# Optimization experiments

Measured on AMD Instinct MI355X. Metric: run time of the kernel, lower is better.

Reference implementation:

```python
import jax, jax.numpy as jnp
import numpy as np

N_NODES = 100000
N_EDGES = 1600000
D_FEAT = 64
D_OUT = 64


def setup_inputs() -> dict:
    key = jax.random.key(0)
    ks = jax.random.split(key, 8)
    return {
        "feat": jax.random.normal(ks[0], (N_NODES, D_FEAT), dtype=jnp.float32),
        "emb": jax.random.normal(ks[1], (N_NODES, D_OUT), dtype=jnp.float32),
        "W1": jax.random.normal(ks[2], (D_OUT, D_FEAT), dtype=jnp.float32) * 0.1,
        "b1": jax.random.normal(ks[3], (D_OUT,), dtype=jnp.float32) * 0.1,
        "W2": jax.random.normal(ks[4], (D_OUT, D_OUT), dtype=jnp.float32) * 0.1,
        "b2": jax.random.normal(ks[5], (D_OUT,), dtype=jnp.float32) * 0.1,
        "edge_src": jax.random.randint(ks[6], (N_EDGES,), 0, N_NODES, dtype=jnp.int32),
        "edge_dst": jax.random.randint(ks[7], (N_EDGES,), 0, N_NODES, dtype=jnp.int32),
    }


def reference(feat, emb, W1, b1, W2, b2, edge_src, edge_dst):
    # n2v: per-node neighbor embedding sum (vectorized gather + segment-sum)
    n_nodes = feat.shape[0]
    nbr_sum = jax.ops.segment_sum(emb[edge_src], edge_dst, num_segments=n_nodes)  # [N, D_OUT]
    new_emb = jax.nn.relu(feat @ W1.T + b1 + nbr_sum @ W2.T + b2)  # [N, D_OUT]
    # g2v: graph embedding = sum of node embeddings
    graph_emb = new_emb.sum(axis=0)  # [D_OUT]
    return graph_emb
```

## Files before the change

kernel.cpp:

```cpp
#include <hip/hip_runtime.h>

#define N_NODES 100000
#define N_EDGES 1600000
#define D 64
#define CAP 32
#define OVF_CAP 8192
#define N_TILES 1563
#define NR 8
#define SLICE_EDGES 2048
#define N_SLICES 782
#define R1_BLOCKS 64
#define R1_ROWS 25
#define ASTRIDE 136

#define NB2 782
#define BCAP2 2560
#define EPB 8192
#define P1_BLOCKS 196
#define CVT_BLOCKS 64

typedef int    vint4  __attribute__((ext_vector_type(4)));
typedef short  s16x4  __attribute__((ext_vector_type(4)));
typedef short  s16x8  __attribute__((ext_vector_type(8)));
typedef float  f32x2  __attribute__((ext_vector_type(2)));
typedef float  f32x4  __attribute__((ext_vector_type(4)));
typedef __bf16 bf16x8 __attribute__((ext_vector_type(8)));

__device__ inline short f2bf(float f) {
    unsigned u = __builtin_bit_cast(unsigned, f);
    u += 0x7fffu + ((u >> 16) & 1u);
    return (short)(u >> 16);
}
__device__ inline s16x4 f2bf4(float4 v) {
    s16x4 r; r.x = f2bf(v.x); r.y = f2bf(v.y); r.z = f2bf(v.z); r.w = f2bf(v.w);
    return r;
}

#define WS_SLOTS_OFF 401408
#define WS_ACC_OFF   13201408
#define WS_OVFC_OFF  38801408
#define WS_OVF_OFF   38801424
#define WS_PART_OFF  38867200
#define WS_PART2_OFF 39267328
#define WS_EMB16_OFF 39283712
#define WS_NEEDED    (WS_PART2_OFF + R1_BLOCKS * 64 * 4)
#define WS_NEEDED16  (WS_EMB16_OFF + N_NODES * D * 2)

__global__ __launch_bounds__(512) void part_kernel(
    const int* __restrict__ edge_src, const int* __restrict__ edge_dst,
    int* __restrict__ bcnt, int* __restrict__ bkt,
    int* __restrict__ ovf_cnt, int2* __restrict__ ovf,
    const float* __restrict__ emb, unsigned* __restrict__ emb8) {
    const int tid = threadIdx.x;
    if (blockIdx.x >= P1_BLOCKS) {
        const float4* e4 = (const float4*)emb;
        const unsigned t0 = (blockIdx.x - P1_BLOCKS) * 512 + tid;
        for (unsigned j = t0; j < (unsigned)(N_NODES * D / 4);
             j += CVT_BLOCKS * 512) {
            float4 v = e4[j];
            int w = 0;
            w = __builtin_amdgcn_cvt_pk_fp8_f32(v.x, v.y, w, false);
            w = __builtin_amdgcn_cvt_pk_fp8_f32(v.z, v.w, w, true);
            emb8[j] = (unsigned)w;
        }
        return;
    }

    __shared__ int stage[EPB];
    __shared__ unsigned short bid[EPB];
    __shared__ int scA[1024];
    __shared__ int scB[1024];
    __shared__ int hist[NB2];
    int* const cur   = scB;
    int* const gbase = scA;

    const int e0 = blockIdx.x * EPB;
    for (int i = tid; i < NB2; i += 512) hist[i] = 0;
    __syncthreads();

    int ss[16], dd[16];
#pragma unroll
    for (int i = 0; i < 16; ++i) {
        const int e = e0 + i * 512 + tid;
        if (e < N_EDGES) { ss[i] = edge_src[e]; dd[i] = edge_dst[e]; }
        else             { ss[i] = 0; dd[i] = -1; }
    }

#pragma unroll
    for (int i = 0; i < 16; ++i)
        if (dd[i] >= 0) atomicAdd(&hist[dd[i] >> 7], 1);
    __syncthreads();

    scA[tid]       = (tid < NB2) ? hist[tid] : 0;
    scA[tid + 512] = 0;
    if (tid + 512 < NB2) scA[tid + 512] = hist[tid + 512];
    __syncthreads();
    {
        int* sA = scA;
        int* sB = scB;
        for (int off = 1; off < 1024; off <<= 1) {
            const int i1 = tid + 512;
            const int v0 = sA[tid] + ((tid >= off) ? sA[tid - off] : 0);
            const int v1 = sA[i1] + sA[i1 - off];
            sB[tid] = v0; sB[i1] = v1;
            __syncthreads();
            int* t = sA; sA = sB; sB = t;
        }
    }
    const int tot = scA[NB2 - 1];
    for (int i = tid; i < NB2; i += 512) cur[i] = scA[i] - hist[i];
    __syncthreads();

#pragma unroll
    for (int i = 0; i < 16; ++i) {
        if (dd[i] >= 0) {
            const int b = dd[i] >> 7;
            const int pos = atomicAdd(&cur[b], 1);
            stage[pos] = (ss[i] << 7) | (dd[i] & 127);
            bid[pos] = (unsigned short)b;
        }
    }
    for (int i = tid; i < NB2; i += 512)
        gbase[i] = atomicAdd(&bcnt[i], hist[i]);
    __syncthreads();

    for (int j = tid; j < tot; j += 512) {
        const int pk = stage[j];
        const int b  = bid[j];
        const int gpos = gbase[b] + (j - (cur[b] - hist[b]));
        if (gpos < BCAP2) {
            bkt[b * BCAP2 + gpos] = pk;
        } else {
            int oj = atomicAdd(ovf_cnt, 1);
            if (oj < OVF_CAP) ovf[oj] = make_int2(pk >> 7, (b << 7) | (pk & 127));
        }
    }
}

__global__ __launch_bounds__(512) void fill2_kernel(
    const int* __restrict__ bcnt, const int* __restrict__ bkt,
    int* __restrict__ cnt, int* __restrict__ slots,
    int* __restrict__ ovf_cnt, int2* __restrict__ ovf) {
    __shared__ int lcnt[128];
    const int b = blockIdx.x;
    const int tid = threadIdx.x;
    if (tid < 128) lcnt[tid] = 0;
    __syncthreads();
    int n = bcnt[b];
    if (n > BCAP2) n = BCAP2;
    for (int i = tid; i < n; i += 512) {
        const int pk = bkt[b * BCAP2 + i];
        const int dl = pk & 127;
        const int pos = atomicAdd(&lcnt[dl], 1);
        const int v = (b << 7) | dl;
        if (pos < CAP) {
            slots[v * CAP + pos] = pk >> 7;
        } else {
            int j = atomicAdd(ovf_cnt, 1);
            if (j < OVF_CAP) ovf[j] = make_int2(pk >> 7, v);
        }
    }
    __syncthreads();
    if (tid < 128) {
        const int v = (b << 7) | tid;
        if (v < N_NODES) cnt[v] = lcnt[tid];
    }
}

__global__ __launch_bounds__(256) void gather8_kernel(
    const unsigned* __restrict__ emb8, const int* __restrict__ cnt,
    const int* __restrict__ slots, float* __restrict__ acc) {
    const int lane = threadIdx.x & 63;
    const int wave = threadIdx.x >> 6;
    const int v = blockIdx.x * 4 + wave;
    const int q = lane >> 4;
    const int c = lane & 15;
    int deg = cnt[v];
    if (deg > CAP) deg = CAP;
    const int si = slots[v * CAP + (lane & (CAP - 1))];

    float4 sum = make_float4(0.f, 0.f, 0.f, 0.f);
    for (int e = 0; e < deg; e += 8) {
        const int i0 = e + q, i1 = e + 4 + q;
        const int s0 = __shfl(si, i0 & (CAP - 1));
        const int s1 = __shfl(si, i1 & (CAP - 1));
        unsigned x0 = 0u, x1 = 0u;
        if (i0 < deg) x0 = emb8[(unsigned)s0 * 16 + c];
        if (i1 < deg) x1 = emb8[(unsigned)s1 * 16 + c];
        const f32x2 a0 = __builtin_amdgcn_cvt_pk_f32_fp8((int)x0, false);
        const f32x2 a1 = __builtin_amdgcn_cvt_pk_f32_fp8((int)x0, true);
        const f32x2 b0 = __builtin_amdgcn_cvt_pk_f32_fp8((int)x1, false);
        const f32x2 b1 = __builtin_amdgcn_cvt_pk_f32_fp8((int)x1, true);
        sum.x += a0.x + b0.x;
        sum.y += a0.y + b0.y;
        sum.z += a1.x + b1.x;
        sum.w += a1.y + b1.y;
    }
#pragma unroll
    for (int off = 16; off < 64; off <<= 1) {
        sum.x += __shfl_xor(sum.x, off);
        sum.y += __shfl_xor(sum.y, off);
        sum.z += __shfl_xor(sum.z, off);
        sum.w += __shfl_xor(sum.w, off);
    }
    if (q == 0) {
        ((float4*)acc)[v * 16 + c] = sum;
    }
}

__global__ __launch_bounds__(256) void fill_kernel(
    const int* __restrict__ edge_src, const int* __restrict__ edge_dst,
    int* __restrict__ cnt, int* __restrict__ slots,
    int* __restrict__ ovf_cnt, int2* __restrict__ ovf) {
    const int r = blockIdx.x & (NR - 1);
    if (r == 7) return;
    const int slice = blockIdx.x >> 3;
    const int base_e = slice * SLICE_EDGES + threadIdx.x * 8;
    if (base_e >= N_EDGES) return;
    const vint4* s4 = (const vint4*)(edge_src + base_e);
    const vint4* d4 = (const vint4*)(edge_dst + base_e);
    vint4 a0 = __builtin_nontemporal_load(s4);
    vint4 a1 = __builtin_nontemporal_load(s4 + 1);
    vint4 b0 = __builtin_nontemporal_load(d4);
    vint4 b1 = __builtin_nontemporal_load(d4 + 1);
    int ss[8] = {a0.x, a0.y, a0.z, a0.w, a1.x, a1.y, a1.z, a1.w};
    int dd[8] = {b0.x, b0.y, b0.z, b0.w, b1.x, b1.y, b1.z, b1.w};
    int pos[8];
#pragma unroll
    for (int i = 0; i < 8; ++i) {
        pos[i] = ((dd[i] >> 14) == r) ? atomicAdd(&cnt[dd[i]], 1) : -1;
    }
#pragma unroll
    for (int i = 0; i < 8; ++i) {
        if (pos[i] >= 0 && pos[i] < CAP) slots[dd[i] * CAP + pos[i]] = ss[i];
    }
#pragma unroll
    for (int i = 0; i < 8; ++i) {
        if (pos[i] >= CAP) {
            int j = atomicAdd(ovf_cnt, 1);
            if (j < OVF_CAP) ovf[j] = make_int2(ss[i], dd[i]);
        }
    }
}

__global__ __launch_bounds__(256) void gather_kernel(
    const float* __restrict__ emb, const int* __restrict__ cnt,
    const int* __restrict__ slots, float* __restrict__ acc) {
    const int lane = threadIdx.x & 63;
    const int wave = threadIdx.x >> 6;
    const int v = blockIdx.x * 4 + wave;
    const int q  = lane >> 4;
    const int c4 = lane & 15;
    int deg = cnt[v];
    if (deg > CAP) deg = CAP;
    const int si = slots[v * CAP + (lane & (CAP - 1))];
    const float4* emb4 = (const float4*)emb;

    float4 sum = make_float4(0.f, 0.f, 0.f, 0.f);
    for (int e = 0; e < deg; e += 4) {
        const int idx = e + q;
        const int s = __shfl(si, idx & (CAP - 1));
        if (idx < deg) {
            float4 a = emb4[s * 16 + c4];
            sum.x += a.x; sum.y += a.y; sum.z += a.z; sum.w += a.w;
        }
    }
#pragma unroll
    for (int off = 16; off < 64; off <<= 1) {
        sum.x += __shfl_xor(sum.x, off);
        sum.y += __shfl_xor(sum.y, off);
        sum.z += __shfl_xor(sum.z, off);
        sum.w += __shfl_xor(sum.w, off);
    }
    if (q == 0) {
        ((float4*)acc)[v * 16 + c4] = sum;
    }
}

__global__ __launch_bounds__(256) void ovf_kernel(
    const float* __restrict__ emb, const int* __restrict__ ovf_cnt,
    const int2* __restrict__ ovf, float* __restrict__ acc) {
    int n = *ovf_cnt;
    if (n > OVF_CAP) n = OVF_CAP;
    const int lane = threadIdx.x & 63;
    const int wv = (blockIdx.x * 256 + threadIdx.x) >> 6;
    const int nwaves = (gridDim.x * 256) >> 6;
    for (int i = wv; i < n; i += nwaves) {
        int2 e = ovf[i];
        unsafeAtomicAdd(&acc[e.y * D + lane], emb[e.x * D + lane]);
    }
}

__global__ __launch_bounds__(256) void scatter_kernel(
    const float* __restrict__ emb,
    const int* __restrict__ edge_src, const int* __restrict__ edge_dst,
    float* __restrict__ acc) {
    int gid = blockIdx.x * 256 + threadIdx.x;
    int e = gid >> 6;
    int c = gid & 63;
    unsafeAtomicAdd(&acc[edge_dst[e] * D + c], emb[edge_src[e] * D + c]);
}

__global__ __launch_bounds__(256) void final_kernel(
    const float* __restrict__ feat, const float* __restrict__ acc,
    const float* __restrict__ W1, const float* __restrict__ b1,
    const float* __restrict__ W2, const float* __restrict__ b2,
    float* __restrict__ partials) {
    __shared__ short A_s[64 * ASTRIDE];
    __shared__ short W_s[64 * ASTRIDE];
    __shared__ float red[4][64];

    const int tid  = threadIdx.x;
    const int lane = tid & 63;
    const int wave = tid >> 6;
    const int quad = lane >> 4;
    const int col  = lane & 15;
    const int node0 = blockIdx.x * 64;

    float bias[4];
#pragma unroll
    for (int nb = 0; nb < 4; ++nb) {
        const int o = nb * 16 + col;
        bias[nb] = b1[o] + b2[o];
    }

    {
        const float4* W1v = (const float4*)W1;
        const float4* W2v = (const float4*)W2;
#pragma unroll
        for (int i = 0; i < 4; ++i) {
            const int flat = tid + i * 256;
            const int row = flat >> 4, c4 = flat & 15;
            *(s16x4*)&W_s[row * ASTRIDE + c4 * 4]      = f2bf4(W1v[flat]);
            *(s16x4*)&W_s[row * ASTRIDE + 64 + c4 * 4] = f2bf4(W2v[flat]);
        }
    }

    {
        const float4* fv = (const float4*)feat;
        const float4* av = (const float4*)acc;
#pragma unroll
        for (int i = 0; i < 4; ++i) {
            const int flat = tid + i * 256;
            const int row = flat >> 4, c4 = flat & 15;
            const int node = node0 + row;
            float4 f = make_float4(0.f, 0.f, 0.f, 0.f);
            float4 n = make_float4(0.f, 0.f, 0.f, 0.f);
            if (node < N_NODES) {
                f = fv[(size_t)node * 16 + c4];
                n = av[(size_t)node * 16 + c4];
            }
            *(s16x4*)&A_s[row * ASTRIDE + c4 * 4]      = f2bf4(f);
            *(s16x4*)&A_s[row * ASTRIDE + 64 + c4 * 4] = f2bf4(n);
        }
    }
    __syncthreads();

    bf16x8 Bf[4][4];
#pragma unroll
    for (int nb = 0; nb < 4; ++nb)
#pragma unroll
        for (int ks = 0; ks < 4; ++ks)
            Bf[nb][ks] = __builtin_bit_cast(bf16x8,
                *(const s16x8*)&W_s[(nb * 16 + col) * ASTRIDE + ks * 32 + quad * 8]);

    f32x4 C[4];
#pragma unroll
    for (int nb = 0; nb < 4; ++nb) C[nb] = (f32x4){0.f, 0.f, 0.f, 0.f};
#pragma unroll
    for (int ks = 0; ks < 4; ++ks) {
        const bf16x8 Af = __builtin_bit_cast(bf16x8,
            *(const s16x8*)&A_s[(wave * 16 + col) * ASTRIDE + ks * 32 + quad * 8]);
#pragma unroll
        for (int nb = 0; nb < 4; ++nb)
            C[nb] = __builtin_amdgcn_mfma_f32_16x16x32_bf16(Af, Bf[nb][ks],
                                                            C[nb], 0, 0, 0);
    }

    float sums[4] = {0.f, 0.f, 0.f, 0.f};
#pragma unroll
    for (int nb = 0; nb < 4; ++nb) {
#pragma unroll
        for (int reg = 0; reg < 4; ++reg) {
            const int node = node0 + wave * 16 + quad * 4 + reg;
            float u = C[nb][reg] + bias[nb];
            u = (u > 0.f) ? u : 0.f;
            if (node < N_NODES) sums[nb] += u;
        }
        sums[nb] += __shfl_xor(sums[nb], 16);
        sums[nb] += __shfl_xor(sums[nb], 32);
        if (lane < 16) red[wave][nb * 16 + lane] = sums[nb];
    }
    __syncthreads();
    if (tid < 64) {
        partials[blockIdx.x * 64 + tid] =
            red[0][tid] + red[1][tid] + red[2][tid] + red[3][tid];
    }
}

__global__ __launch_bounds__(256) void reduce1_kernel(
    const float* __restrict__ partials, float* __restrict__ part2) {
    __shared__ float red[4][64];
    const int col = threadIdx.x & 63;
    const int seg = threadIdx.x >> 6;
    const int r0 = blockIdx.x * R1_ROWS;
    int r1 = r0 + R1_ROWS;
    if (r1 > N_TILES) r1 = N_TILES;
    float s = 0.f;
    for (int r = r0 + seg; r < r1; r += 4) s += partials[r * 64 + col];
    red[seg][col] = s;
    __syncthreads();
    if (seg == 0) {
        part2[blockIdx.x * 64 + col] =
            red[0][col] + red[1][col] + red[2][col] + red[3][col];
    }
}

__global__ __launch_bounds__(256) void reduce2_kernel(
    const float* __restrict__ part2, float* __restrict__ out) {
    __shared__ float red[4][64];
    const int col = threadIdx.x & 63;
    const int seg = threadIdx.x >> 6;
    float s = 0.f;
    for (int r = seg; r < R1_BLOCKS; r += 4) s += part2[r * 64 + col];
    red[seg][col] = s;
    __syncthreads();
    if (seg == 0) {
        out[col] = red[0][col] + red[1][col] + red[2][col] + red[3][col];
    }
}

extern "C" void kernel_launch(void* const* d_in, const int* in_sizes, int n_in,
                              void* d_out, int out_size, void* d_ws, size_t ws_size,
                              hipStream_t stream) {
    const float* feat = (const float*)d_in[0];
    const float* emb  = (const float*)d_in[1];
    const float* W1   = (const float*)d_in[2];
    const float* b1   = (const float*)d_in[3];
    const float* W2   = (const float*)d_in[4];
    const float* b2   = (const float*)d_in[5];
    const int* edge_src = (const int*)d_in[6];
    const int* edge_dst = (const int*)d_in[7];
    float* out = (float*)d_out;
    char* ws = (char*)d_ws;

    if (ws_size >= (size_t)WS_NEEDED16) {
        int*      cnt      = (int*)ws;
        int*      slots    = (int*)(ws + WS_SLOTS_OFF);
        float*    acc      = (float*)(ws + WS_ACC_OFF);
        int*      bkt      = (int*)(ws + WS_ACC_OFF);
        int*      ovf_cnt  = (int*)(ws + WS_OVFC_OFF);
        int2*     ovf      = (int2*)(ws + WS_OVF_OFF);
        float*    partials = (float*)(ws + WS_PART_OFF);
        int*      bcnt     = (int*)(ws + WS_PART_OFF);
        float*    part2    = (float*)(ws + WS_PART2_OFF);
        unsigned* emb8     = (unsigned*)(ws + WS_EMB16_OFF);

        (void)hipMemsetAsync(ovf_cnt, 0, sizeof(int), stream);
        (void)hipMemsetAsync(bcnt, 0, NB2 * sizeof(int), stream);

        part_kernel<<<P1_BLOCKS + CVT_BLOCKS, 512, 0, stream>>>(
            edge_src, edge_dst, bcnt, bkt, ovf_cnt, ovf, emb, emb8);
        fill2_kernel<<<NB2, 512, 0, stream>>>(bcnt, bkt, cnt, slots,
                                              ovf_cnt, ovf);
        gather8_kernel<<<N_NODES / 4, 256, 0, stream>>>(emb8, cnt, slots, acc);
        ovf_kernel<<<16, 256, 0, stream>>>(emb, ovf_cnt, ovf, acc);

        final_kernel<<<N_TILES, 256, 0, stream>>>(feat, acc, W1, b1, W2, b2,
                                                  partials);
        reduce1_kernel<<<R1_BLOCKS, 256, 0, stream>>>(partials, part2);
        reduce2_kernel<<<1, 256, 0, stream>>>(part2, out);
    } else if (ws_size >= (size_t)WS_NEEDED) {
        int*   cnt      = (int*)ws;
        int*   slots    = (int*)(ws + WS_SLOTS_OFF);
        float* acc      = (float*)(ws + WS_ACC_OFF);
        int*   ovf_cnt  = (int*)(ws + WS_OVFC_OFF);
        int2*  ovf      = (int2*)(ws + WS_OVF_OFF);
        float* partials = (float*)(ws + WS_PART_OFF);
        float* part2    = (float*)(ws + WS_PART2_OFF);

        (void)hipMemsetAsync(cnt, 0, N_NODES * sizeof(int), stream);
        (void)hipMemsetAsync(ovf_cnt, 0, sizeof(int), stream);

        fill_kernel<<<NR * N_SLICES, 256, 0, stream>>>(edge_src, edge_dst,
                                                       cnt, slots, ovf_cnt, ovf);
        gather_kernel<<<N_NODES / 4, 256, 0, stream>>>(emb, cnt, slots, acc);
        ovf_kernel<<<16, 256, 0, stream>>>(emb, ovf_cnt, ovf, acc);

        final_kernel<<<N_TILES, 256, 0, stream>>>(feat, acc, W1, b1, W2, b2,
                                                  partials);
        reduce1_kernel<<<R1_BLOCKS, 256, 0, stream>>>(partials, part2);
        reduce2_kernel<<<1, 256, 0, stream>>>(part2, out);
    } else {
        float* acc = (float*)ws;
        (void)hipMemsetAsync(acc, 0, (size_t)N_NODES * D * sizeof(float), stream);
        scatter_kernel<<<(N_EDGES * 64) / 256, 256, 0, stream>>>(emb, edge_src,
                                                                 edge_dst, acc);
        float* partials = (float*)(ws + (size_t)N_NODES * D * sizeof(float));
        float* part2    = partials + (size_t)N_TILES * 64;
        final_kernel<<<N_TILES, 256, 0, stream>>>(feat, acc, W1, b1, W2, b2,
                                                  partials);
        reduce1_kernel<<<R1_BLOCKS, 256, 0, stream>>>(partials, part2);
        reduce2_kernel<<<1, 256, 0, stream>>>(part2, out);
    }
}
```

Before: 186.3 us.

## Store neighbor sums and features as bf16 and pre-convert weights for final GEMM

The gather kernel now writes neighbor sums as bf16 instead of fp32, and feat plus the concatenated W1/W2 are converted to bf16 in the spare conversion blocks of the partition kernel, which grows from 64 to 128 blocks. A new final kernel loads these pre-packed bf16 tiles directly rather than converting fp32 inputs itself. Overflow edges are now applied by a single serial 64-thread block doing read-modify-write in bf16. The aim is to cut the memory traffic of the acc write and the final-kernel reads, at the cost of an extra feat conversion pass, a serial overflow path and some precision loss.

```diff
diff --git a/kernel.cpp b/kernel.cpp
--- a/kernel.cpp
+++ b/kernel.cpp
@@ -17,7 +17,7 @@
 #define BCAP2 2560
 #define EPB 8192
 #define P1_BLOCKS 196
-#define CVT_BLOCKS 64
+#define CVT_BLOCKS 128
 
 typedef int    vint4  __attribute__((ext_vector_type(4)));
 typedef short  s16x4  __attribute__((ext_vector_type(4)));
@@ -35,33 +35,69 @@
     s16x4 r; r.x = f2bf(v.x); r.y = f2bf(v.y); r.z = f2bf(v.z); r.w = f2bf(v.w);
     return r;
 }
-
-#define WS_SLOTS_OFF 401408
-#define WS_ACC_OFF   13201408
-#define WS_OVFC_OFF  38801408
-#define WS_OVF_OFF   38801424
-#define WS_PART_OFF  38867200
-#define WS_PART2_OFF 39267328
-#define WS_EMB16_OFF 39283712
-#define WS_NEEDED    (WS_PART2_OFF + R1_BLOCKS * 64 * 4)
-#define WS_NEEDED16  (WS_EMB16_OFF + N_NODES * D * 2)
+__device__ inline float bf2f(short s) {
+    return __builtin_bit_cast(float, ((unsigned)(unsigned short)s) << 16);
+}
+
+#define WS_SLOTS_OFF  401408
+#define WS_ACC_OFF    13201408
+#define WS_ACC16_OFF  13201408
+#define WS_FEAT16_OFF 26001408
+#define WS_OVFC_OFF   38801408
+#define WS_OVF_OFF    38801424
+#define WS_PART_OFF   38867200
+#define WS_PART2_OFF  39267328
+#define WS_EMB8_OFF   39283712
+#define WS_W16_OFF    45683712
+#define WS_NEEDED     (WS_PART2_OFF + R1_BLOCKS * 64 * 4)
+#define WS_NEEDED16   (WS_W16_OFF + 64 * 128 * 2)
 
 __global__ __launch_bounds__(512) void part_kernel(
     const int* __restrict__ edge_src, const int* __restrict__ edge_dst,
     int* __restrict__ bcnt, int* __restrict__ bkt,
     int* __restrict__ ovf_cnt, int2* __restrict__ ovf,
-    const float* __restrict__ emb, unsigned* __restrict__ emb8) {
+    const float* __restrict__ emb, unsigned* __restrict__ emb8,
+    const float* __restrict__ feat, short* __restrict__ feat16,
+    const float* __restrict__ W1, const float* __restrict__ W2,
+    short* __restrict__ w16) {
     const int tid = threadIdx.x;
     if (blockIdx.x >= P1_BLOCKS) {
-        const float4* e4 = (const float4*)emb;
-        const unsigned t0 = (blockIdx.x - P1_BLOCKS) * 512 + tid;
-        for (unsigned j = t0; j < (unsigned)(N_NODES * D / 4);
-             j += CVT_BLOCKS * 512) {
-            float4 v = e4[j];
-            int w = 0;
-            w = __builtin_amdgcn_cvt_pk_fp8_f32(v.x, v.y, w, false);
-            w = __builtin_amdgcn_cvt_pk_fp8_f32(v.z, v.w, w, true);
-            emb8[j] = (unsigned)w;
+        const int rid = blockIdx.x - P1_BLOCKS;
+        {
+            const float4* e4 = (const float4*)emb;
+            for (unsigned j = rid * 512 + tid; j < (unsigned)(N_NODES * D / 4);
+                 j += CVT_BLOCKS * 512) {
+                float4 v = e4[j];
+                int w = 0;
+                w = __builtin_amdgcn_cvt_pk_fp8_f32(v.x, v.y, w, false);
+                w = __builtin_amdgcn_cvt_pk_fp8_f32(v.z, v.w, w, true);
+                emb8[j] = (unsigned)w;
+            }
+        }
+        {
+            const float4* f4 = (const float4*)feat;
+            for (unsigned k = rid * 512 + tid; k < (unsigned)(N_NODES * D / 8);
+                 k += CVT_BLOCKS * 512) {
+                float4 a = f4[k * 2];
+                float4 b = f4[k * 2 + 1];
+                s16x4 lo = f2bf4(a), hi = f2bf4(b);
+                s16x8 pk = {lo.x, lo.y, lo.z, lo.w, hi.x, hi.y, hi.z, hi.w};
+                *(s16x8*)&feat16[k * 8] = pk;
+            }
+        }
+        if (rid == 0) {
+            const float4* W1v = (const float4*)W1;
+            const float4* W2v = (const float4*)W2;
+            for (int k = tid; k < 64 * 16; k += 512) {
+                const int row = k >> 4, c = k & 15;
+                const float4 a = (c < 8) ? W1v[row * 16 + c * 2]
+                                         : W2v[row * 16 + (c - 8) * 2];
+                const float4 b = (c < 8) ? W1v[row * 16 + c * 2 + 1]
+                                         : W2v[row * 16 + (c - 8) * 2 + 1];
+                s16x4 lo = f2bf4(a), hi = f2bf4(b);
+                s16x8 pk = {lo.x, lo.y, lo.z, lo.w, hi.x, hi.y, hi.z, hi.w};
+                *(s16x8*)&w16[row * 128 + c * 8] = pk;
+            }
         }
         return;
     }
@@ -169,7 +205,7 @@
 
 __global__ __launch_bounds__(256) void gather8_kernel(
     const unsigned* __restrict__ emb8, const int* __restrict__ cnt,
-    const int* __restrict__ slots, float* __restrict__ acc) {
+    const int* __restrict__ slots, short* __restrict__ acc16) {
     const int lane = threadIdx.x & 63;
     const int wave = threadIdx.x >> 6;
     const int v = blockIdx.x * 4 + wave;
@@ -204,7 +240,20 @@
         sum.w += __shfl_xor(sum.w, off);
     }
     if (q == 0) {
-        ((float4*)acc)[v * 16 + c] = sum;
+        *(s16x4*)&acc16[v * D + c * 4] = f2bf4(sum);
+    }
+}
+
+__global__ __launch_bounds__(64) void ovf2_kernel(
+    const float* __restrict__ emb, const int* __restrict__ ovf_cnt,
+    const int2* __restrict__ ovf, short* __restrict__ acc16) {
+    int n = *ovf_cnt;
+    if (n > OVF_CAP) n = OVF_CAP;
+    const int l = threadIdx.x;
+    for (int i = 0; i < n; ++i) {
+        const int2 e = ovf[i];
+        const float a = bf2f(acc16[e.y * D + l]) + emb[e.x * D + l];
+        acc16[e.y * D + l] = f2bf(a);
     }
 }
 
@@ -301,6 +350,91 @@
     unsafeAtomicAdd(&acc[edge_dst[e] * D + c], emb[edge_src[e] * D + c]);
 }
 
+__global__ __launch_bounds__(256) void final16_kernel(
+    const short* __restrict__ feat16, const short* __restrict__ acc16,
+    const short* __restrict__ w16, const float* __restrict__ b1,
+    const float* __restrict__ b2, float* __restrict__ partials) {
+    __shared__ short A_s[64 * ASTRIDE];
+    __shared__ short W_s[64 * ASTRIDE];
+    __shared__ float red[4][64];
+
+    const int tid  = threadIdx.x;
+    const int lane = tid & 63;
+    const int wave = tid >> 6;
+    const int quad = lane >> 4;
+    const int col  = lane & 15;
+    const int node0 = blockIdx.x * 64;
+
+    float bias[4];
+#pragma unroll
+    for (int nb = 0; nb < 4; ++nb) {
+        const int o = nb * 16 + col;
+        bias[nb] = b1[o] + b2[o];
+    }
+
+#pragma unroll
+    for (int i = 0; i < 4; ++i) {
+        const int flat = tid + i * 256;
+        const int row = flat >> 4, c = flat & 15;
+        *(s16x8*)&W_s[row * ASTRIDE + c * 8] = *(const s16x8*)&w16[flat * 8];
+    }
+
+#pragma unroll
+    for (int i = 0; i < 4; ++i) {
+        const int flat = tid + i * 256;
+        const int row = flat >> 4, c = flat & 15;
+        const int node = node0 + row;
+        s16x8 pk = {0, 0, 0, 0, 0, 0, 0, 0};
+        if (node < N_NODES) {
+            pk = (c < 8) ? *(const s16x8*)&feat16[node * D + c * 8]
+                         : *(const s16x8*)&acc16[node * D + (c - 8) * 8];
+        }
+        *(s16x8*)&A_s[row * ASTRIDE + c * 8] = pk;
+    }
+    __syncthreads();
+
+    bf16x8 Bf[4][4];
+#pragma unroll
+    for (int nb = 0; nb < 4; ++nb)
+#pragma unroll
+        for (int ks = 0; ks < 4; ++ks)
+            Bf[nb][ks] = __builtin_bit_cast(bf16x8,
+                *(const s16x8*)&W_s[(nb * 16 + col) * ASTRIDE + ks * 32 + quad * 8]);
+
+    f32x4 C[4];
+#pragma unroll
+    for (int nb = 0; nb < 4; ++nb) C[nb] = (f32x4){0.f, 0.f, 0.f, 0.f};
+#pragma unroll
+    for (int ks = 0; ks < 4; ++ks) {
+        const bf16x8 Af = __builtin_bit_cast(bf16x8,
+            *(const s16x8*)&A_s[(wave * 16 + col) * ASTRIDE + ks * 32 + quad * 8]);
+#pragma unroll
+        for (int nb = 0; nb < 4; ++nb)
+            C[nb] = __builtin_amdgcn_mfma_f32_16x16x32_bf16(Af, Bf[nb][ks],
+                                                            C[nb], 0, 0, 0);
+    }
+
+    float sums[4] = {0.f, 0.f, 0.f, 0.f};
+#pragma unroll
+    for (int nb = 0; nb < 4; ++nb) {
+#pragma unroll
+        for (int reg = 0; reg < 4; ++reg) {
+            const int node = node0 + wave * 16 + quad * 4 + reg;
+            float u = C[nb][reg] + bias[nb];
+            u = (u > 0.f) ? u : 0.f;
+            if (node < N_NODES) sums[nb] += u;
+        }
+        sums[nb] += __shfl_xor(sums[nb], 16);
+        sums[nb] += __shfl_xor(sums[nb], 32);
+        if (lane < 16) red[wave][nb * 16 + lane] = sums[nb];
+    }
+    __syncthreads();
+    if (tid < 64) {
+        partials[blockIdx.x * 64 + tid] =
+            red[0][tid] + red[1][tid] + red[2][tid] + red[3][tid];
+    }
+}
+
 __global__ __launch_bounds__(256) void final_kernel(
     const float* __restrict__ feat, const float* __restrict__ acc,
     const float* __restrict__ W1, const float* __restrict__ b1,
@@ -447,27 +581,30 @@
     if (ws_size >= (size_t)WS_NEEDED16) {
         int*      cnt      = (int*)ws;
         int*      slots    = (int*)(ws + WS_SLOTS_OFF);
-        float*    acc      = (float*)(ws + WS_ACC_OFF);
-        int*      bkt      = (int*)(ws + WS_ACC_OFF);
+        short*    acc16    = (short*)(ws + WS_ACC16_OFF);
+        int*      bkt      = (int*)(ws + WS_ACC16_OFF);
+        short*    feat16   = (short*)(ws + WS_FEAT16_OFF);
         int*      ovf_cnt  = (int*)(ws + WS_OVFC_OFF);
         int2*     ovf      = (int2*)(ws + WS_OVF_OFF);
         float*    partials = (float*)(ws + WS_PART_OFF);
         int*      bcnt     = (int*)(ws + WS_PART_OFF);
         float*    part2    = (float*)(ws + WS_PART2_OFF);
-        unsigned* emb8     = (unsigned*)(ws + WS_EMB16_OFF);
+        unsigned* emb8     = (unsigned*)(ws + WS_EMB8_OFF);
+        short*    w16      = (short*)(ws + WS_W16_OFF);
 
         (void)hipMemsetAsync(ovf_cnt, 0, sizeof(int), stream);
         (void)hipMemsetAsync(bcnt, 0, NB2 * sizeof(int), stream);
 
         part_kernel<<<P1_BLOCKS + CVT_BLOCKS, 512, 0, stream>>>(
-            edge_src, edge_dst, bcnt, bkt, ovf_cnt, ovf, emb, emb8);
+            edge_src, edge_dst, bcnt, bkt, ovf_cnt, ovf,
+            emb, emb8, feat, feat16, W1, W2, w16);
         fill2_kernel<<<NB2, 512, 0, stream>>>(bcnt, bkt, cnt, slots,
                                               ovf_cnt, ovf);
-        gather8_kernel<<<N_NODES / 4, 256, 0, stream>>>(emb8, cnt, slots, acc);
-        ovf_kernel<<<16, 256, 0, stream>>>(emb, ovf_cnt, ovf, acc);
-
-        final_kernel<<<N_TILES, 256, 0, stream>>>(feat, acc, W1, b1, W2, b2,
-                                                  partials);
+        gather8_kernel<<<N_NODES / 4, 256, 0, stream>>>(emb8, cnt, slots, acc16);
+        ovf2_kernel<<<1, 64, 0, stream>>>(emb, ovf_cnt, ovf, acc16);
+
+        final16_kernel<<<N_TILES, 256, 0, stream>>>(feat16, acc16, w16,
+                                                    b1, b2, partials);
         reduce1_kernel<<<R1_BLOCKS, 256, 0, stream>>>(partials, part2);
         reduce2_kernel<<<1, 256, 0, stream>>>(part2, out);
     } else if (ws_size >= (size_t)WS_NEEDED) {
```

After: 197.6 us. 1.06x slower.
